# Optimization experiments

Hardware: AMD Instinct MI355X
Metric: run time of the kernel (lower is better)

The kernel has to match this reference:

```python
import jax, jax.numpy as jnp
import numpy as np

N = 50000
E = 800000
IN_C, HID, OUT_C, HEADS = 128, 32, 64, 4
NEG_SLOPE = 0.2


def setup_inputs() -> dict:
    key = jax.random.key(0)
    ks = jax.random.split(key, 10)
    x = jax.random.normal(ks[0], (N, IN_C), dtype=jnp.float32)
    edge_index = jax.random.randint(ks[1], (2, E), 0, N, dtype=jnp.int64)
    s = 0.05
    W1 = jax.random.normal(ks[2], (IN_C, HID), dtype=jnp.float32) * s
    b1 = jnp.zeros((HID,), dtype=jnp.float32)
    Wg = jax.random.normal(ks[3], (HID, HEADS * HID), dtype=jnp.float32) * s
    ag_src = jax.random.normal(ks[4], (HEADS, HID), dtype=jnp.float32) * s
    ag_dst = jax.random.normal(ks[5], (HEADS, HID), dtype=jnp.float32) * s
    bg = jnp.zeros((HID,), dtype=jnp.float32)
    W2 = jax.random.normal(ks[6], (HID, OUT_C), dtype=jnp.float32) * s
    b2 = jnp.zeros((OUT_C,), dtype=jnp.float32)
    return {"x": x, "edge_index": edge_index, "W1": W1, "b1": b1,
            "Wg": Wg, "ag_src": ag_src, "ag_dst": ag_dst, "bg": bg,
            "W2": W2, "b2": b2}


def _add_self_loops(edge_index, n):
    loop = jnp.arange(n, dtype=edge_index.dtype)
    return jnp.concatenate([edge_index, jnp.stack([loop, loop])], axis=1)


def _gcn(x, src, dst, W, b, n):
    # PyG GCNConv: symmetric normalization with self-loops, scatter-add
    xw = x @ W  # [N, F]
    deg = jnp.zeros((n,), xw.dtype).at[dst].add(1.0)  # in-degree incl self-loops
    dinv = jax.lax.rsqrt(deg)
    norm = dinv[src] * dinv[dst]  # [E']
    msg = xw[src] * norm[:, None]  # [E', F]
    out = jax.ops.segment_sum(msg, dst, num_segments=n)
    return out + b


def _gat(x, src, dst, Wg, a_src, a_dst, b, n):
    # PyG GATConv, concat=False (mean over heads), leaky_relu slope 0.2
    h = (x @ Wg).reshape(n, HEADS, HID)  # [N, H, D]
    al_s = jnp.einsum('nhd,hd->nh', h, a_src)  # [N, H]
    al_d = jnp.einsum('nhd,hd->nh', h, a_dst)
    logits = jax.nn.leaky_relu(al_s[src] + al_d[dst], NEG_SLOPE)  # [E', H]
    # segment softmax over incoming edges of each dst node
    m = jax.ops.segment_max(logits, dst, num_segments=n)
    e = jnp.exp(logits - m[dst])
    denom = jax.ops.segment_sum(e, dst, num_segments=n)
    alpha = e / denom[dst]  # [E', H]
    msg = h[src] * alpha[:, :, None]  # [E', H, D]
    out = jax.ops.segment_sum(msg, dst, num_segments=n)  # [N, H, D]
    return out.mean(axis=1) + b


def reference(x, edge_index, W1, b1, Wg, ag_src, ag_dst, bg, W2, b2):
    ei = _add_self_loops(edge_index, N)
    src, dst = ei[0], ei[1]
    h = jax.nn.relu(_gcn(x, src, dst, W1, b1, N))
    h = jax.nn.relu(_gat(h, src, dst, Wg, ag_src, ag_dst, bg, N))
    return _gcn(h, src, dst, W2, b2, N)
```

## Files before the change

### kernel.cpp

```cpp
#include <hip/hip_runtime.h>
#include <hip/hip_bf16.h>

#define N_NODES 50000
#define N_EDGES 800000
#define IN_C 128
#define HID 32
#define OUT_C 64
#define HEADS 4
#define NEG_SLOPE 0.2f

#define MAXDEG 64
#define N_PART 8
#define PART_W ((N_NODES + N_PART - 1) / N_PART)
#define SC_BLOCKS 2048
#define RANKS (SC_BLOCKS / N_PART)
#define EPB ((N_EDGES + RANKS - 1) / RANKS)

typedef unsigned int uint32;
typedef unsigned short u16;
typedef __attribute__((ext_vector_type(8))) short bf16x8;
typedef __attribute__((ext_vector_type(4))) float f32x4;

__device__ __forceinline__ float bf_lo(uint32 u) { return __uint_as_float(u << 16); }
__device__ __forceinline__ float bf_hi(uint32 u) { return __uint_as_float(u & 0xffff0000u); }
__device__ __forceinline__ uint32 f2bf(float f) {
    uint32 u = __float_as_uint(f);
    return (u + 0x7fffu + ((u >> 16) & 1u)) >> 16;
}
__device__ __forceinline__ uint32 pack_bf2(float a, float b) {
    return f2bf(a) | (f2bf(b) << 16);
}

__global__ __launch_bounds__(256) void k_scatter(const int* __restrict__ ei,
                                                 int* __restrict__ ncnt,
                                                 u16* __restrict__ srcs_pad,
                                                 const float* __restrict__ Wg,
                                                 const float* __restrict__ ags,
                                                 const float* __restrict__ agd,
                                                 float* __restrict__ wals,
                                                 float* __restrict__ wald,
                                                 const float* __restrict__ W2,
                                                 uint32* __restrict__ wgB,
                                                 uint32* __restrict__ w2B) {
    int t = threadIdx.x;
    int part = blockIdx.x & (N_PART - 1);
    int rank = blockIdx.x >> 3;
    int lo = part * PART_W;
    int e0 = rank * EPB;
    int e1 = e0 + EPB; if (e1 > N_EDGES) e1 = N_EDGES;
    for (int e = e0 + t; e < e1; e += 256) {
        int d = ei[N_EDGES + e];
        if ((uint32)(d - lo) < (uint32)PART_W) {
            int s = ei[e];
            int pos = atomicAdd(&ncnt[d], 1);
            if (pos < MAXDEG) srcs_pad[(d << 6) + pos] = (u16)s;
        }
    }
    if (blockIdx.x == 0) {
        {
            int c = t & 127;
            int h = c >> 5, k = c & 31;
            const float* a = (t < 128) ? ags : agd;
            float acc = 0.f;
#pragma unroll
            for (int d = 0; d < 32; d++) acc += Wg[k * 128 + h * 32 + d] * a[h * 32 + d];
            if (t < 128) wals[c] = acc; else wald[c] = acc;
        }
        for (int i = t; i < 2048; i += 256) {
            int tile = i >> 8;
            int T = tile >> 2, kt = tile & 3;
            int r = i & 255;
            int L = r >> 2, di = r & 3;
            int k0 = kt * 32 + (L >> 4) * 8 + 2 * di;
            int k1 = k0 + 1;
            int n = T * 16 + (L & 15);
            float a = Wg[(k0 & 31) * 128 + (k0 >> 5) * 32 + n];
            float b = Wg[(k1 & 31) * 128 + (k1 >> 5) * 32 + n];
            wgB[i] = pack_bf2(a, b);
        }
        for (int i = t; i < 1024; i += 256) {
            int T = i >> 8;
            int r = i & 255;
            int L = r >> 2, di = r & 3;
            int k0 = (L >> 4) * 8 + 2 * di;
            int n = T * 16 + (L & 15);
            w2B[i] = pack_bf2(W2[k0 * 64 + n], W2[(k0 + 1) * 64 + n]);
        }
    }
}

__global__ __launch_bounds__(256) void k_gemm1(const float* __restrict__ x,
                                               const float* __restrict__ W1,
                                               const int* __restrict__ ncnt,
                                               uint32* __restrict__ xw1) {
    __shared__ float wl[IN_C * HID];
    __shared__ float xl[8 * IN_C];
    int t = threadIdx.x;
    for (int i = t; i < IN_C * HID; i += 256) {
        int k = i >> 5, f = i & 31;
        wl[(k >> 1) * 64 + f * 2 + (k & 1)] = W1[i];
    }
    int nb = blockIdx.x * 8;
    const float4* x4 = (const float4*)(x + (size_t)nb * IN_C);
    ((float4*)xl)[t] = x4[t];
    __syncthreads();
    int g = t >> 5, f = t & 31;
    const float2* xr = (const float2*)(xl + g * IN_C);
    const float2* wp = (const float2*)wl;
    float acc = 0.f;
#pragma unroll 16
    for (int k2 = 0; k2 < 64; k2++) {
        float2 xv = xr[k2];
        float2 wv = wp[k2 * 32 + f];
        acc += xv.x * wv.x + xv.y * wv.y;
    }
    float v = acc * rsqrtf((float)(ncnt[nb + g] + 1));
    float vn = __shfl_xor(v, 1, 64);
    if ((f & 1) == 0) xw1[(size_t)(nb + g) * 16 + (f >> 1)] = pack_bf2(v, vn);
}

__global__ __launch_bounds__(256) void k_gather1(const uint32* __restrict__ xw1,
                                                 const int* __restrict__ ncnt,
                                                 const u16* __restrict__ srcs_pad,
                                                 const float* __restrict__ b1,
                                                 const float* __restrict__ wals,
                                                 const float* __restrict__ wald,
                                                 char* __restrict__ recH,
                                                 float* __restrict__ als,
                                                 float* __restrict__ ald) {
    __shared__ u16 s_src[16 * 64];
    int t = threadIdx.x;
    {
        const uint32* gsrc = (const uint32*)(srcs_pad + ((size_t)blockIdx.x * 16 << 6));
        ((uint32*)s_src)[t] = gsrc[t];
        ((uint32*)s_src)[t + 256] = gsrc[t + 256];
    }
    __syncthreads();
    int l16 = t & 15;
    int es = l16 >> 2;
    int q  = l16 & 3;
    int n = blockIdx.x * 16 + (t >> 4);
    int sbase = (t >> 4) << 6;
    int deg = ncnt[n];
    float a0 = 0.f, a1 = 0.f, a2 = 0.f, a3 = 0.f;
    float a4 = 0.f, a5 = 0.f, a6 = 0.f, a7 = 0.f;
#pragma unroll 2
    for (int jb = 0; jb <= deg; jb += 4) {
        int je = jb + es;
        if (je <= deg) {
            int sidx = (je < deg) ? (int)s_src[sbase + je] : n;
            uint4 u = *(const uint4*)((const char*)xw1 + ((uint32)sidx << 6) + q * 16);
            a0 += bf_lo(u.x); a1 += bf_hi(u.x);
            a2 += bf_lo(u.y); a3 += bf_hi(u.y);
            a4 += bf_lo(u.z); a5 += bf_hi(u.z);
            a6 += bf_lo(u.w); a7 += bf_hi(u.w);
        }
    }
#define RED_ES(v) v += __shfl_xor(v, 4, 64); v += __shfl_xor(v, 8, 64);
    RED_ES(a0) RED_ES(a1) RED_ES(a2) RED_ES(a3)
    RED_ES(a4) RED_ES(a5) RED_ES(a6) RED_ES(a7)
#undef RED_ES
    float dn = rsqrtf((float)(deg + 1));
    float4 bA = ((const float4*)b1)[2 * q];
    float4 bB = ((const float4*)b1)[2 * q + 1];
    float v0 = a0 * dn + bA.x, v1 = a1 * dn + bA.y;
    float v2 = a2 * dn + bA.z, v3 = a3 * dn + bA.w;
    float v4 = a4 * dn + bB.x, v5 = a5 * dn + bB.y;
    float v6 = a6 * dn + bB.z, v7 = a7 * dn + bB.w;
    v0 = v0 > 0.f ? v0 : 0.f; v1 = v1 > 0.f ? v1 : 0.f;
    v2 = v2 > 0.f ? v2 : 0.f; v3 = v3 > 0.f ? v3 : 0.f;
    v4 = v4 > 0.f ? v4 : 0.f; v5 = v5 > 0.f ? v5 : 0.f;
    v6 = v6 > 0.f ? v6 : 0.f; v7 = v7 > 0.f ? v7 : 0.f;
    if (es == 0) {
        uint4 w;
        w.x = pack_bf2(v0, v1); w.y = pack_bf2(v2, v3);
        w.z = pack_bf2(v4, v5); w.w = pack_bf2(v6, v7);
        *(uint4*)(recH + ((uint32)n << 6) + q * 16) = w;
    }
    float ps[4], pd[4];
#pragma unroll
    for (int h = 0; h < 4; h++) {
        const float4* wa = (const float4*)(wals + h * 32 + 8 * q);
        float4 wv0 = wa[0], wv1 = wa[1];
        ps[h] = v0 * wv0.x + v1 * wv0.y + v2 * wv0.z + v3 * wv0.w
              + v4 * wv1.x + v5 * wv1.y + v6 * wv1.z + v7 * wv1.w;
        const float4* wb = (const float4*)(wald + h * 32 + 8 * q);
        float4 uv0 = wb[0], uv1 = wb[1];
        pd[h] = v0 * uv0.x + v1 * uv0.y + v2 * uv0.z + v3 * uv0.w
              + v4 * uv1.x + v5 * uv1.y + v6 * uv1.z + v7 * uv1.w;
    }
#pragma unroll
    for (int h = 0; h < 4; h++) {
        ps[h] += __shfl_xor(ps[h], 1, 64); ps[h] += __shfl_xor(ps[h], 2, 64);
        pd[h] += __shfl_xor(pd[h], 1, 64); pd[h] += __shfl_xor(pd[h], 2, 64);
    }
    if (l16 == 0) {
        ((float4*)als)[n] = make_float4(ps[0], ps[1], ps[2], ps[3]);
        ((float4*)ald)[n] = make_float4(pd[0], pd[1], pd[2], pd[3]);
    }
}

__global__ __launch_bounds__(512) void k_gat_agg(const char* __restrict__ recH,
                                                 const float* __restrict__ als,
                                                 const float* __restrict__ ald,
                                                 const int* __restrict__ ncnt,
                                                 const u16* __restrict__ srcs_pad,
                                                 const uint32* __restrict__ wgB,
                                                 const float* __restrict__ bg,
                                                 uint32* __restrict__ h2s) {
    __shared__ __align__(16) uint32 gl[16][64];
    __shared__ u16 s_src[16 * 64];
    int t = threadIdx.x;
    {
        const uint32* gsrc = (const uint32*)(srcs_pad + ((size_t)blockIdx.x * 16 << 6));
        ((uint32*)s_src)[t] = gsrc[t];
    }
    __syncthreads();
    int l32 = t & 31;
    int g8 = t >> 5;
    int n = blockIdx.x * 16 + g8;
    int es = l32 >> 3;
    int q  = l32 & 7;
    int sbase = g8 << 6;
    int deg = ncnt[n];
    float4 dv = ((const float4*)ald)[n];

    float g00 = 0.f, g01 = 0.f, g02 = 0.f, g03 = 0.f;
    float g10 = 0.f, g11 = 0.f, g12 = 0.f, g13 = 0.f;
    float g20 = 0.f, g21 = 0.f, g22 = 0.f, g23 = 0.f;
    float g30 = 0.f, g31 = 0.f, g32 = 0.f, g33 = 0.f;
    float ss0 = 0.f, ss1 = 0.f, ss2 = 0.f, ss3 = 0.f;

#pragma unroll 2
    for (int jb = 0; jb <= deg; jb += 4) {
        int je = jb + es;
        if (je <= deg) {
            int sidx = (je < deg) ? (int)s_src[sbase + je] : n;
            float4 ev = ((const float4*)als)[sidx];
            uint2 u = *(const uint2*)(recH + ((uint32)sidx << 6) + q * 8);
            float f0 = bf_lo(u.x), f1 = bf_hi(u.x);
            float f2 = bf_lo(u.y), f3 = bf_hi(u.y);
            float tt, w;
            tt = ev.x + dv.x; w = __expf(fmaxf(tt, NEG_SLOPE * tt));
            ss0 += w; g00 += w * f0; g01 += w * f1; g02 += w * f2; g03 += w * f3;
            tt = ev.y + dv.y; w = __expf(fmaxf(tt, NEG_SLOPE * tt));
            ss1 += w; g10 += w * f0; g11 += w * f1; g12 += w * f2; g13 += w * f3;
            tt = ev.z + dv.z; w = __expf(fmaxf(tt, NEG_SLOPE * tt));
            ss2 += w; g20 += w * f0; g21 += w * f1; g22 += w * f2; g23 += w * f3;
            tt = ev.w + dv.w; w = __expf(fmaxf(tt, NEG_SLOPE * tt));
            ss3 += w; g30 += w * f0; g31 += w * f1; g32 += w * f2; g33 += w * f3;
        }
    }
#define RED_ES(v) v += __shfl_xor(v, 8, 64); v += __shfl_xor(v, 16, 64);
    RED_ES(ss0) RED_ES(ss1) RED_ES(ss2) RED_ES(ss3)
    RED_ES(g00) RED_ES(g01) RED_ES(g02) RED_ES(g03)
    RED_ES(g10) RED_ES(g11) RED_ES(g12) RED_ES(g13)
    RED_ES(g20) RED_ES(g21) RED_ES(g22) RED_ES(g23)
    RED_ES(g30) RED_ES(g31) RED_ES(g32) RED_ES(g33)
#undef RED_ES
    float i0 = 0.25f / ss0, i1 = 0.25f / ss1, i2 = 0.25f / ss2, i3 = 0.25f / ss3;
    if (es == 0) {
        uint2 w;
        w.x = pack_bf2(g00 * i0, g01 * i0); w.y = pack_bf2(g02 * i0, g03 * i0);
        *(uint2*)&gl[g8][0 * 16 + 2 * q] = w;
        w.x = pack_bf2(g10 * i1, g11 * i1); w.y = pack_bf2(g12 * i1, g13 * i1);
        *(uint2*)&gl[g8][1 * 16 + 2 * q] = w;
        w.x = pack_bf2(g20 * i2, g21 * i2); w.y = pack_bf2(g22 * i2, g23 * i2);
        *(uint2*)&gl[g8][2 * 16 + 2 * q] = w;
        w.x = pack_bf2(g30 * i3, g31 * i3); w.y = pack_bf2(g32 * i3, g33 * i3);
        *(uint2*)&gl[g8][3 * 16 + 2 * q] = w;
    }
    __syncthreads();
    if (t < 64) {
        int L = t;
        int mA = L & 15;
        int quad = L >> 4;
        int nbase = blockIdx.x * 16;
        float dns[4];
#pragma unroll
        for (int r = 0; r < 4; r++)
            dns[r] = rsqrtf((float)(ncnt[nbase + quad * 4 + r] + 1));
#pragma unroll
        for (int T = 0; T < 2; T++) {
            f32x4 acc = {0.f, 0.f, 0.f, 0.f};
#pragma unroll
            for (int kt = 0; kt < 4; kt++) {
                bf16x8 af = *(const bf16x8*)&gl[mA][kt * 16 + quad * 4];
                bf16x8 bf = *(const bf16x8*)(wgB + (size_t)((T * 4 + kt) * 64 + L) * 4);
                acc = __builtin_amdgcn_mfma_f32_16x16x32_bf16(af, bf, acc, 0, 0, 0);
            }
            int d = T * 16 + (L & 15);
            float bgd = bg[d];
#pragma unroll
            for (int r = 0; r < 4; r++) {
                int node = nbase + quad * 4 + r;
                float v = acc[r] + bgd;
                v = v > 0.f ? v : 0.f;
                v *= dns[r];
                float vn = __shfl_xor(v, 1, 64);
                if ((d & 1) == 0)
                    h2s[(size_t)node * 16 + (d >> 1)] = pack_bf2(v, vn);
            }
        }
    }
}

__global__ __launch_bounds__(256) void k_gather2(const uint32* __restrict__ h2s,
                                                 const int* __restrict__ ncnt,
                                                 const u16* __restrict__ srcs_pad,
                                                 const uint32* __restrict__ w2B,
                                                 const float* __restrict__ b2,
                                                 float* __restrict__ out) {
    __shared__ __align__(16) uint32 gbf[16][16];
    __shared__ u16 s_src[16 * 64];
    int t = threadIdx.x;
    {
        const uint32* gsrc = (const uint32*)(srcs_pad + ((size_t)blockIdx.x * 16 << 6));
        ((uint32*)s_src)[t] = gsrc[t];
        ((uint32*)s_src)[t + 256] = gsrc[t + 256];
    }
    __syncthreads();
    int l16 = t & 15;
    int es = l16 >> 2;
    int q  = l16 & 3;
    int g16 = t >> 4;
    int n = blockIdx.x * 16 + g16;
    int sbase = g16 << 6;
    int deg = ncnt[n];
    float a0 = 0.f, a1 = 0.f, a2 = 0.f, a3 = 0.f;
    float a4 = 0.f, a5 = 0.f, a6 = 0.f, a7 = 0.f;
#pragma unroll 2
    for (int jb = 0; jb <= deg; jb += 4) {
        int je = jb + es;
        if (je <= deg) {
            int sidx = (je < deg) ? (int)s_src[sbase + je] : n;
            uint4 u = *(const uint4*)((const char*)h2s + ((uint32)sidx << 6) + q * 16);
            a0 += bf_lo(u.x); a1 += bf_hi(u.x);
            a2 += bf_lo(u.y); a3 += bf_hi(u.y);
            a4 += bf_lo(u.z); a5 += bf_hi(u.z);
            a6 += bf_lo(u.w); a7 += bf_hi(u.w);
        }
    }
#define RED_ES(v) v += __shfl_xor(v, 4, 64); v += __shfl_xor(v, 8, 64);
    RED_ES(a0) RED_ES(a1) RED_ES(a2) RED_ES(a3)
    RED_ES(a4) RED_ES(a5) RED_ES(a6) RED_ES(a7)
#undef RED_ES
    if (es == 0) {
        uint4 w;
        w.x = pack_bf2(a0, a1); w.y = pack_bf2(a2, a3);
        w.z = pack_bf2(a4, a5); w.w = pack_bf2(a6, a7);
        *(uint4*)&gbf[g16][4 * q] = w;
    }
    __syncthreads();
    if (t < 64) {
        int L = t;
        int quad = L >> 4;
        int nbase = blockIdx.x * 16;
        float dns[4];
#pragma unroll
        for (int r = 0; r < 4; r++)
            dns[r] = rsqrtf((float)(ncnt[nbase + quad * 4 + r] + 1));
        bf16x8 af = *(const bf16x8*)&gbf[L & 15][quad * 4];
#pragma unroll
        for (int T = 0; T < 4; T++) {
            bf16x8 bf = *(const bf16x8*)(w2B + (size_t)(T * 64 + L) * 4);
            f32x4 acc = {0.f, 0.f, 0.f, 0.f};
            acc = __builtin_amdgcn_mfma_f32_16x16x32_bf16(af, bf, acc, 0, 0, 0);
            int d = T * 16 + (L & 15);
            float b2d = b2[d];
#pragma unroll
            for (int r = 0; r < 4; r++) {
                int node = nbase + quad * 4 + r;
                out[(size_t)node * OUT_C + d] = acc[r] * dns[r] + b2d;
            }
        }
    }
}

extern "C" void kernel_launch(void* const* d_in, const int* in_sizes, int n_in,
                              void* d_out, int out_size, void* d_ws, size_t ws_size,
                              hipStream_t stream) {
    const float* x   = (const float*)d_in[0];
    const int*   ei  = (const int*)d_in[1];
    const float* W1  = (const float*)d_in[2];
    const float* b1  = (const float*)d_in[3];
    const float* Wg  = (const float*)d_in[4];
    const float* ags = (const float*)d_in[5];
    const float* agd = (const float*)d_in[6];
    const float* bg  = (const float*)d_in[7];
    const float* W2  = (const float*)d_in[8];
    const float* b2  = (const float*)d_in[9];
    float* out = (float*)d_out;

    char* p = (char*)d_ws;
    auto alloc = [&](size_t bytes) -> void* {
        void* r = (void*)p;
        p += (bytes + 255) & ~(size_t)255;
        return r;
    };
    int*    ncnt     = (int*)   alloc((size_t)N_NODES * 4);
    u16*    srcs_pad = (u16*)   alloc((size_t)N_NODES * MAXDEG * 2);
    uint32* xw1      = (uint32*)alloc((size_t)N_NODES * 16 * 4);
    char*   recH     = (char*)  alloc((size_t)N_NODES * 64);
    float*  als      = (float*) alloc((size_t)N_NODES * 4 * 4);
    float*  ald      = (float*) alloc((size_t)N_NODES * 4 * 4);
    float*  wals     = (float*) alloc(128 * 4);
    float*  wald     = (float*) alloc(128 * 4);
    uint32* wgB      = (uint32*)alloc(2048 * 4);
    uint32* w2B      = (uint32*)alloc(1024 * 4);
    uint32* h2s      = (uint32*)alloc((size_t)N_NODES * 16 * 4);

    hipMemsetAsync(ncnt, 0, (size_t)N_NODES * 4, stream);

    k_scatter<<<SC_BLOCKS, 256, 0, stream>>>(
        ei, ncnt, srcs_pad, Wg, ags, agd, wals, wald, W2, wgB, w2B);

    k_gemm1<<<N_NODES / 8, 256, 0, stream>>>(x, W1, ncnt, xw1);

    k_gather1<<<N_NODES / 16, 256, 0, stream>>>(xw1, ncnt, srcs_pad, b1,
                                                wals, wald, recH, als, ald);

    k_gat_agg<<<N_NODES / 16, 512, 0, stream>>>(recH, als, ald, ncnt, srcs_pad,
                                                wgB, bg, h2s);

    k_gather2<<<N_NODES / 16, 256, 0, stream>>>(h2s, ncnt, srcs_pad, w2B, b2, out);
}
```

Before: 216.5 us.

## Fuse edge scatter and first GEMM into one launch, defer source normalization

Merges the edge-bucketing scatter kernel and the first dense projection into a single grid, with block ranges split between the two roles, so they can run concurrently. The GEMM no longer depends on degree counts, so the source-side rsqrt(deg) scale moves into the first gather, which now loads each neighbor's count per edge. This removes one kernel boundary and lets compute-bound GEMM blocks overlap with the atomic-bound scatter. In exchange the gather does an extra random 4-byte load and rsqrt per edge.

```diff
diff --git a/kernel.cpp b/kernel.cpp
--- a/kernel.cpp
+++ b/kernel.cpp
@@ -15,6 +15,7 @@
 #define SC_BLOCKS 2048
 #define RANKS (SC_BLOCKS / N_PART)
 #define EPB ((N_EDGES + RANKS - 1) / RANKS)
+#define GEMM1_BLOCKS (N_NODES / 8)
 
 typedef unsigned int uint32;
 typedef unsigned short u16;
@@ -31,92 +32,92 @@
     return f2bf(a) | (f2bf(b) << 16);
 }
 
-__global__ __launch_bounds__(256) void k_scatter(const int* __restrict__ ei,
-                                                 int* __restrict__ ncnt,
-                                                 u16* __restrict__ srcs_pad,
-                                                 const float* __restrict__ Wg,
-                                                 const float* __restrict__ ags,
-                                                 const float* __restrict__ agd,
-                                                 float* __restrict__ wals,
-                                                 float* __restrict__ wald,
-                                                 const float* __restrict__ W2,
-                                                 uint32* __restrict__ wgB,
-                                                 uint32* __restrict__ w2B) {
-    int t = threadIdx.x;
-    int part = blockIdx.x & (N_PART - 1);
-    int rank = blockIdx.x >> 3;
-    int lo = part * PART_W;
-    int e0 = rank * EPB;
-    int e1 = e0 + EPB; if (e1 > N_EDGES) e1 = N_EDGES;
-    for (int e = e0 + t; e < e1; e += 256) {
-        int d = ei[N_EDGES + e];
-        if ((uint32)(d - lo) < (uint32)PART_W) {
-            int s = ei[e];
-            int pos = atomicAdd(&ncnt[d], 1);
-            if (pos < MAXDEG) srcs_pad[(d << 6) + pos] = (u16)s;
-        }
-    }
-    if (blockIdx.x == 0) {
-        {
-            int c = t & 127;
-            int h = c >> 5, k = c & 31;
-            const float* a = (t < 128) ? ags : agd;
-            float acc = 0.f;
-#pragma unroll
-            for (int d = 0; d < 32; d++) acc += Wg[k * 128 + h * 32 + d] * a[h * 32 + d];
-            if (t < 128) wals[c] = acc; else wald[c] = acc;
-        }
-        for (int i = t; i < 2048; i += 256) {
-            int tile = i >> 8;
-            int T = tile >> 2, kt = tile & 3;
-            int r = i & 255;
-            int L = r >> 2, di = r & 3;
-            int k0 = kt * 32 + (L >> 4) * 8 + 2 * di;
-            int k1 = k0 + 1;
-            int n = T * 16 + (L & 15);
-            float a = Wg[(k0 & 31) * 128 + (k0 >> 5) * 32 + n];
-            float b = Wg[(k1 & 31) * 128 + (k1 >> 5) * 32 + n];
-            wgB[i] = pack_bf2(a, b);
-        }
-        for (int i = t; i < 1024; i += 256) {
-            int T = i >> 8;
-            int r = i & 255;
-            int L = r >> 2, di = r & 3;
-            int k0 = (L >> 4) * 8 + 2 * di;
-            int n = T * 16 + (L & 15);
-            w2B[i] = pack_bf2(W2[k0 * 64 + n], W2[(k0 + 1) * 64 + n]);
-        }
-    }
-}
-
-__global__ __launch_bounds__(256) void k_gemm1(const float* __restrict__ x,
-                                               const float* __restrict__ W1,
-                                               const int* __restrict__ ncnt,
-                                               uint32* __restrict__ xw1) {
+__global__ __launch_bounds__(256) void k_fused1(const float* __restrict__ ei_x,
+                                                const int* __restrict__ ei,
+                                                int* __restrict__ ncnt,
+                                                u16* __restrict__ srcs_pad,
+                                                const float* __restrict__ W1,
+                                                uint32* __restrict__ xw1,
+                                                const float* __restrict__ Wg,
+                                                const float* __restrict__ ags,
+                                                const float* __restrict__ agd,
+                                                float* __restrict__ wals,
+                                                float* __restrict__ wald,
+                                                const float* __restrict__ W2,
+                                                uint32* __restrict__ wgB,
+                                                uint32* __restrict__ w2B) {
     __shared__ float wl[IN_C * HID];
     __shared__ float xl[8 * IN_C];
     int t = threadIdx.x;
-    for (int i = t; i < IN_C * HID; i += 256) {
-        int k = i >> 5, f = i & 31;
-        wl[(k >> 1) * 64 + f * 2 + (k & 1)] = W1[i];
-    }
-    int nb = blockIdx.x * 8;
-    const float4* x4 = (const float4*)(x + (size_t)nb * IN_C);
-    ((float4*)xl)[t] = x4[t];
-    __syncthreads();
-    int g = t >> 5, f = t & 31;
-    const float2* xr = (const float2*)(xl + g * IN_C);
-    const float2* wp = (const float2*)wl;
-    float acc = 0.f;
+    if (blockIdx.x < GEMM1_BLOCKS) {
+        const float* x = ei_x;
+        for (int i = t; i < IN_C * HID; i += 256) {
+            int k = i >> 5, f = i & 31;
+            wl[(k >> 1) * 64 + f * 2 + (k & 1)] = W1[i];
+        }
+        int nb = blockIdx.x * 8;
+        const float4* x4 = (const float4*)(x + (size_t)nb * IN_C);
+        ((float4*)xl)[t] = x4[t];
+        __syncthreads();
+        int g = t >> 5, f = t & 31;
+        const float2* xr = (const float2*)(xl + g * IN_C);
+        const float2* wp = (const float2*)wl;
+        float acc = 0.f;
 #pragma unroll 16
-    for (int k2 = 0; k2 < 64; k2++) {
-        float2 xv = xr[k2];
-        float2 wv = wp[k2 * 32 + f];
-        acc += xv.x * wv.x + xv.y * wv.y;
-    }
-    float v = acc * rsqrtf((float)(ncnt[nb + g] + 1));
-    float vn = __shfl_xor(v, 1, 64);
-    if ((f & 1) == 0) xw1[(size_t)(nb + g) * 16 + (f >> 1)] = pack_bf2(v, vn);
+        for (int k2 = 0; k2 < 64; k2++) {
+            float2 xv = xr[k2];
+            float2 wv = wp[k2 * 32 + f];
+            acc += xv.x * wv.x + xv.y * wv.y;
+        }
+        float vn = __shfl_xor(acc, 1, 64);
+        if ((f & 1) == 0) xw1[(size_t)(nb + g) * 16 + (f >> 1)] = pack_bf2(acc, vn);
+        if (blockIdx.x == 0) {
+            {
+                int c = t & 127;
+                int h = c >> 5, k = c & 31;
+                const float* a = (t < 128) ? ags : agd;
+                float acc2 = 0.f;
+#pragma unroll
+                for (int d = 0; d < 32; d++) acc2 += Wg[k * 128 + h * 32 + d] * a[h * 32 + d];
+                if (t < 128) wals[c] = acc2; else wald[c] = acc2;
+            }
+            for (int i = t; i < 2048; i += 256) {
+                int tile = i >> 8;
+                int T = tile >> 2, kt = tile & 3;
+                int r = i & 255;
+                int L = r >> 2, di = r & 3;
+                int k0 = kt * 32 + (L >> 4) * 8 + 2 * di;
+                int k1 = k0 + 1;
+                int n = T * 16 + (L & 15);
+                float a = Wg[(k0 & 31) * 128 + (k0 >> 5) * 32 + n];
+                float b = Wg[(k1 & 31) * 128 + (k1 >> 5) * 32 + n];
+                wgB[i] = pack_bf2(a, b);
+            }
+            for (int i = t; i < 1024; i += 256) {
+                int T = i >> 8;
+                int r = i & 255;
+                int L = r >> 2, di = r & 3;
+                int k0 = (L >> 4) * 8 + 2 * di;
+                int n = T * 16 + (L & 15);
+                w2B[i] = pack_bf2(W2[k0 * 64 + n], W2[(k0 + 1) * 64 + n]);
+            }
+        }
+    } else {
+        int b = blockIdx.x - GEMM1_BLOCKS;
+        int part = b & (N_PART - 1);
+        int rank = b >> 3;
+        int lo = part * PART_W;
+        int e0 = rank * EPB;
+        int e1 = e0 + EPB; if (e1 > N_EDGES) e1 = N_EDGES;
+        for (int e = e0 + t; e < e1; e += 256) {
+            int d = ei[N_EDGES + e];
+            if ((uint32)(d - lo) < (uint32)PART_W) {
+                int s = ei[e];
+                int pos = atomicAdd(&ncnt[d], 1);
+                if (pos < MAXDEG) srcs_pad[(d << 6) + pos] = (u16)s;
+            }
+        }
+    }
 }
 
 __global__ __launch_bounds__(256) void k_gather1(const uint32* __restrict__ xw1,
@@ -149,11 +150,12 @@
         int je = jb + es;
         if (je <= deg) {
             int sidx = (je < deg) ? (int)s_src[sbase + je] : n;
+            float ws = rsqrtf((float)(ncnt[sidx] + 1));
             uint4 u = *(const uint4*)((const char*)xw1 + ((uint32)sidx << 6) + q * 16);
-            a0 += bf_lo(u.x); a1 += bf_hi(u.x);
-            a2 += bf_lo(u.y); a3 += bf_hi(u.y);
-            a4 += bf_lo(u.z); a5 += bf_hi(u.z);
-            a6 += bf_lo(u.w); a7 += bf_hi(u.w);
+            a0 = fmaf(ws, bf_lo(u.x), a0); a1 = fmaf(ws, bf_hi(u.x), a1);
+            a2 = fmaf(ws, bf_lo(u.y), a2); a3 = fmaf(ws, bf_hi(u.y), a3);
+            a4 = fmaf(ws, bf_lo(u.z), a4); a5 = fmaf(ws, bf_hi(u.z), a5);
+            a6 = fmaf(ws, bf_lo(u.w), a6); a7 = fmaf(ws, bf_hi(u.w), a7);
         }
     }
 #define RED_ES(v) v += __shfl_xor(v, 4, 64); v += __shfl_xor(v, 8, 64);
@@ -412,10 +414,9 @@
 
     hipMemsetAsync(ncnt, 0, (size_t)N_NODES * 4, stream);
 
-    k_scatter<<<SC_BLOCKS, 256, 0, stream>>>(
-        ei, ncnt, srcs_pad, Wg, ags, agd, wals, wald, W2, wgB, w2B);
-
-    k_gemm1<<<N_NODES / 8, 256, 0, stream>>>(x, W1, ncnt, xw1);
+    k_fused1<<<GEMM1_BLOCKS + SC_BLOCKS, 256, 0, stream>>>(
+        x, ei, ncnt, srcs_pad, W1, xw1,
+        Wg, ags, agd, wals, wald, W2, wgB, w2B);
 
     k_gather1<<<N_NODES / 16, 256, 0, stream>>>(xw1, ncnt, srcs_pad, b1,
                                                 wals, wald, recH, als, ald);
```

After: 210.3 us. -2.9%, faster.
